# Performance work log

Measured on AMD Instinct MI355X. Metric: run time of the kernel, lower is better.

Reference implementation:

```python
import jax, jax.numpy as jnp
import numpy as np
from jax import lax

# dims: S=seq_len, B=batch, D=word dim, HE=encoder hidden, HD=decoder hidden,
# E=atomic embedding dim, A=num_atomic, T=max_steps, SOS=start token id
S, B, D = 48, 64, 300
HE, HD, E, A, T, SOS = 300, 256, 50, 128, 50, 1


def _u(key, shape, scale):
    return jax.random.uniform(key, shape, jnp.float32, -scale, scale)


def setup_inputs() -> dict:
    key = jax.random.key(0)
    ks = iter(jax.random.split(key, 64))
    inp = {"word_vectors": jax.random.normal(next(ks), (S, B, D), jnp.float32)}
    se = 1.0 / np.sqrt(HE)
    for l, din in ((0, D), (1, 2 * HE)):
        for d in ("f", "b"):
            inp[f"e{l}{d}_Wih"] = _u(next(ks), (3 * HE, din), se)
            inp[f"e{l}{d}_Whh"] = _u(next(ks), (3 * HE, HE), se)
            inp[f"e{l}{d}_bih"] = _u(next(ks), (3 * HE,), se)
            inp[f"e{l}{d}_bhh"] = _u(next(ks), (3 * HE,), se)
    sd = 1.0 / np.sqrt(HD)
    for l, din in ((0, E), (1, HD)):
        inp[f"d{l}_Wih"] = _u(next(ks), (3 * HD, din), sd)
        inp[f"d{l}_Whh"] = _u(next(ks), (3 * HD, HD), sd)
        inp[f"d{l}_bih"] = _u(next(ks), (3 * HD,), sd)
        inp[f"d{l}_bhh"] = _u(next(ks), (3 * HD,), sd)
    emb = jax.random.normal(next(ks), (A, E), jnp.float32)
    inp["emb"] = emb.at[0].set(0.0)  # padding_idx=0
    inp["Wout"] = _u(next(ks), (A, HD), sd)
    inp["bout"] = _u(next(ks), (A,), sd)
    so = 1.0 / np.sqrt(D)
    inp["Wh0"] = _u(next(ks), (2 * HD, D), so)
    inp["bh0"] = _u(next(ks), (2 * HD,), so)
    return inp


def gru_cell(x, h, Wih, Whh, bih, bhh):
    # PyTorch GRU cell semantics
    gi = x @ Wih.T + bih
    gh = h @ Whh.T + bhh
    ir, iz, inn = jnp.split(gi, 3, axis=-1)
    hr, hz, hn = jnp.split(gh, 3, axis=-1)
    r = jax.nn.sigmoid(ir + hr)
    z = jax.nn.sigmoid(iz + hz)
    n = jnp.tanh(inn + r * hn)
    return (1.0 - z) * n + z * h


def gru_layer(xs, Wih, Whh, bih, bhh, reverse=False):
    # xs: [S, B, din] -> [S, B, H]; h0 = zeros (torch default)
    h0 = jnp.zeros((xs.shape[1], Whh.shape[1]), xs.dtype)
    def step(h, x):
        hn = gru_cell(x, h, Wih, Whh, bih, bhh)
        return hn, hn
    _, ys = lax.scan(step, h0, xs, reverse=reverse)
    return ys


def reference(word_vectors, e0f_Wih, e0f_Whh, e0f_bih, e0f_bhh, e0b_Wih, e0b_Whh, e0b_bih, e0b_bhh, e1f_Wih, e1f_Whh, e1f_bih, e1f_bhh, e1b_Wih, e1b_Whh, e1b_bih, e1b_bhh, d0_Wih, d0_Whh, d0_bih, d0_bhh, d1_Wih, d1_Whh, d1_bih, d1_bhh, emb, Wout, bout, Wh0, bh0):
    # --- encoder: 2-layer bidirectional GRU (eval mode: no dropout) ---
    x0f = gru_layer(word_vectors, e0f_Wih, e0f_Whh, e0f_bih, e0f_bhh, reverse=False)
    x0b = gru_layer(word_vectors, e0b_Wih, e0b_Whh, e0b_bih, e0b_bhh, reverse=True)
    x0 = jnp.concatenate([x0f, x0b], axis=-1)  # [S,B,2*HE]
    x1f = gru_layer(x0, e1f_Wih, e1f_Whh, e1f_bih, e1f_bhh, reverse=False)
    x1b = gru_layer(x0, e1b_Wih, e1b_Whh, e1b_bih, e1b_bhh, reverse=True)
    enc = x1f + x1b  # view(S,B,2,HE).sum(dim=2) of concat == sum of directions

    N = S * B
    h = jnp.tanh(enc @ Wh0.T + bh0).reshape(N, 2, HD)  # [N,2,HD]
    h0, h1 = h[:, 0], h[:, 1]
    e = jnp.broadcast_to(emb[SOS], (N, E))

    def step(carry, _):
        h0, h1, e = carry
        h0n = gru_cell(e, h0, d0_Wih, d0_Whh, d0_bih, d0_bhh)
        h1n = gru_cell(h0n, h1, d1_Wih, d1_Whh, d1_bih, d1_bhh)
        y = jax.nn.log_softmax(h1n @ Wout.T + bout, axis=-1)  # [N,A]
        p = jnp.argmax(y, axis=-1)
        return (h0n, h1n, emb[p]), y

    _, Y = lax.scan(step, (h0, h1, e), None, length=T)  # [T,N,A]
    return Y.reshape(T, S, B, A)[:-1]
```

## Files before the change

kernel.cpp:

```cpp
#include <hip/hip_runtime.h>
#include <math.h>

#define S_ 48
#define B_ 64
#define D_ 300
#define HE_ 300
#define HD_ 256
#define E_ 50
#define A_ 128
#define T_ 50
#define N_ (S_*B_)

__device__ __forceinline__ float sigm(float x){ return 1.0f/(1.0f + expf(-x)); }

template<int MODE>
__global__ __launch_bounds__(256)
void gemm_bias_kernel(const float* __restrict__ A, const float* __restrict__ A2,
                      const float* __restrict__ W,
                      const float* __restrict__ bias, float* __restrict__ C,
                      float* __restrict__ C2, int M, int N, int K)
{
  __shared__ float As[16][64];
  __shared__ float Ws[16][64];
  const int tid = threadIdx.x;
  const int bm = blockIdx.y * 64;
  const int bn = blockIdx.x * 64;
  const int tx = tid & 15, ty = tid >> 4;
  const int lr = tid >> 2;
  const int lk = (tid & 3) << 2;
  float acc[4][4] = {{0.f}};
  for (int kb = 0; kb < K; kb += 16) {
    {
      const int row = bm + lr;
      const int k = kb + lk;
      const float* ap = A + (size_t)row * K + k;
      float4 v = make_float4(0.f,0.f,0.f,0.f);
      if (k + 3 < K) v = *reinterpret_cast<const float4*>(ap);
      else {
        if (k   < K) v.x = ap[0];
        if (k+1 < K) v.y = ap[1];
        if (k+2 < K) v.z = ap[2];
        if (k+3 < K) v.w = ap[3];
      }
      if (MODE == 2) {
        const float* ap2 = A2 + (size_t)row * K + k;
        if (k + 3 < K) {
          float4 v2 = *reinterpret_cast<const float4*>(ap2);
          v.x += v2.x; v.y += v2.y; v.z += v2.z; v.w += v2.w;
        } else {
          if (k   < K) v.x += ap2[0];
          if (k+1 < K) v.y += ap2[1];
          if (k+2 < K) v.z += ap2[2];
          if (k+3 < K) v.w += ap2[3];
        }
      }
      As[lk][lr]=v.x; As[lk+1][lr]=v.y; As[lk+2][lr]=v.z; As[lk+3][lr]=v.w;
    }
    {
      const int col = bn + lr;
      const int k = kb + lk;
      float4 v = make_float4(0.f,0.f,0.f,0.f);
      if (col < N) {
        const float* wp = W + (size_t)col * K + k;
        if (k + 3 < K) v = *reinterpret_cast<const float4*>(wp);
        else {
          if (k   < K) v.x = wp[0];
          if (k+1 < K) v.y = wp[1];
          if (k+2 < K) v.z = wp[2];
          if (k+3 < K) v.w = wp[3];
        }
      }
      Ws[lk][lr]=v.x; Ws[lk+1][lr]=v.y; Ws[lk+2][lr]=v.z; Ws[lk+3][lr]=v.w;
    }
    __syncthreads();
    #pragma unroll
    for (int kk = 0; kk < 16; ++kk) {
      float4 a4 = *reinterpret_cast<const float4*>(&As[kk][ty<<2]);
      float4 w4 = *reinterpret_cast<const float4*>(&Ws[kk][tx<<2]);
      const float* a = reinterpret_cast<const float*>(&a4);
      const float* w = reinterpret_cast<const float*>(&w4);
      #pragma unroll
      for (int i = 0; i < 4; ++i)
        #pragma unroll
        for (int j = 0; j < 4; ++j)
          acc[i][j] = fmaf(a[i], w[j], acc[i][j]);
    }
    __syncthreads();
  }
  #pragma unroll
  for (int i = 0; i < 4; ++i) {
    const int m = bm + (ty<<2) + i;
    #pragma unroll
    for (int j = 0; j < 4; ++j) {
      const int n = bn + (tx<<2) + j;
      if (n < N) {
        float v = acc[i][j] + bias[n];
        if (MODE == 0) {
          C[(size_t)m*N + n] = v;
        } else {
          v = tanhf(v);
          if (n < HD_) C[(size_t)m*HD_ + n] = v;
          else         C2[(size_t)m*HD_ + (n-HD_)] = v;
        }
      }
    }
  }
}

__global__ __launch_bounds__(256)
void transpose_kernel(const float* __restrict__ in, float* __restrict__ out,
                      int NC, int NK, int NKP)
{
  int idx = blockIdx.x * 256 + threadIdx.x;
  if (idx < NC*NKP) {
    int cI = idx / NKP, kI = idx % NKP;
    out[(size_t)kI*NC + cI] = (kI < NK) ? in[(size_t)cI*NK + kI] : 0.0f;
  }
}

template<int LAYER>
__global__ __launch_bounds__(640, 2)
void enc_layer_persistent(const float* __restrict__ gi_f, const float* __restrict__ gi_b,
                          const float* __restrict__ WhhT_f, const float* __restrict__ WhhT_b,
                          const float* __restrict__ bhh_f, const float* __restrict__ bhh_b,
                          float* __restrict__ out, float* __restrict__ outB)
{
  const int dir = blockIdx.y;
  const float* gi  = dir ? gi_b   : gi_f;
  const float* WT  = dir ? WhhT_b : WhhT_f;
  const float* bhh = dir ? bhh_b  : bhh_f;
  float* o = (LAYER == 1 && dir) ? outB : out;

  __shared__ float hA[4][304];
  __shared__ float hB[4][304];
  const int tid = threadIdx.x;
  const int half = tid / 320;
  const int j = tid - half*320;
  const int R0 = blockIdx.x * 4;
  const int r0 = half * 2;
  const bool act = (j < HE_);

  float b_r = 0.f, b_z = 0.f, b_n = 0.f;
  if (act) { b_r = bhh[j]; b_z = bhh[HE_+j]; b_n = bhh[2*HE_+j]; }
  __syncthreads();

  for (int t = 0; t < S_; ++t) {
    const int tt = dir ? (S_-1 - t) : t;
    float (*hin)[304]  = (t & 1) ? hB : hA;
    float (*hout)[304] = (t & 1) ? hA : hB;
    float ar[2]={0,0}, az[2]={0,0}, an[2]={0,0};
    if (act && t > 0) {
      for (int k = 0; k < HE_; k += 4) {
        float wr[4], wz[4], wn[4];
        #pragma unroll
        for (int u = 0; u < 4; ++u) {
          const float* wk = WT + (size_t)(k+u)*(3*HE_);
          wr[u] = wk[j]; wz[u] = wk[HE_+j]; wn[u] = wk[2*HE_+j];
        }
        #pragma unroll
        for (int r = 0; r < 2; ++r) {
          float4 h4 = *reinterpret_cast<const float4*>(&hin[r0+r][k]);
          ar[r]=fmaf(h4.x,wr[0],ar[r]); ar[r]=fmaf(h4.y,wr[1],ar[r]);
          ar[r]=fmaf(h4.z,wr[2],ar[r]); ar[r]=fmaf(h4.w,wr[3],ar[r]);
          az[r]=fmaf(h4.x,wz[0],az[r]); az[r]=fmaf(h4.y,wz[1],az[r]);
          az[r]=fmaf(h4.z,wz[2],az[r]); az[r]=fmaf(h4.w,wz[3],az[r]);
          an[r]=fmaf(h4.x,wn[0],an[r]); an[r]=fmaf(h4.y,wn[1],an[r]);
          an[r]=fmaf(h4.z,wn[2],an[r]); an[r]=fmaf(h4.w,wn[3],an[r]);
        }
      }
    }
    if (act) {
      #pragma unroll
      for (int r = 0; r < 2; ++r) {
        const int row = R0 + r0 + r;
        const size_t gb = (size_t)(tt*B_ + row) * (3*HE_);
        float gr = gi[gb + j];
        float gz = gi[gb + HE_ + j];
        float gn = gi[gb + 2*HE_ + j];
        float rg = sigm(gr + ar[r] + b_r);
        float zg = sigm(gz + az[r] + b_z);
        float ng = tanhf(gn + rg*(an[r] + b_n));
        float ho = (t > 0) ? hin[r0+r][j] : 0.0f;
        float hn = (1.0f - zg)*ng + zg*ho;
        hout[r0+r][j] = hn;
        if (LAYER == 0) o[(size_t)(tt*B_ + row)*(2*HE_) + dir*HE_ + j] = hn;
        else            o[(size_t)(tt*B_ + row)*HE_ + j] = hn;
      }
    }
    __syncthreads();
  }
}

__global__ __launch_bounds__(1024, 4)
void dec_persistent(const float* __restrict__ WihT0,
                    const float* __restrict__ WhhT0,
                    const float* __restrict__ WihT1,
                    const float* __restrict__ WhhT1,
                    const float* __restrict__ WoutT,
                    const float* __restrict__ bih0, const float* __restrict__ bhh0,
                    const float* __restrict__ bih1, const float* __restrict__ bhh1,
                    const float* __restrict__ bout,
                    const float* __restrict__ emb,
                    const float* __restrict__ h0init, const float* __restrict__ h1init,
                    float* __restrict__ Y)
{
  __shared__ float h0s[12][256];
  __shared__ float h1s[12][256];
  __shared__ float es[12][52];
  const int tid = threadIdx.x;
  const int R0 = blockIdx.x * 12;
  const int c  = tid & 255;
  const int q  = tid >> 8;
  const int r0 = q * 3;

  for (int i = tid; i < 12*64; i += 1024) {
    int r = i >> 6, k = (i & 63) << 2;
    *reinterpret_cast<float4*>(&h0s[r][k]) =
        *reinterpret_cast<const float4*>(&h0init[(size_t)(R0+r)*HD_ + k]);
    *reinterpret_cast<float4*>(&h1s[r][k]) =
        *reinterpret_cast<const float4*>(&h1init[(size_t)(R0+r)*HD_ + k]);
  }
  for (int i = tid; i < 12*52; i += 1024) {
    int r = i / 52, k = i - r*52;
    es[r][k] = (k < E_) ? emb[E_ + k] : 0.0f;
  }
  const float b0r = bih0[c] + bhh0[c];
  const float b0z = bih0[HD_+c] + bhh0[HD_+c];
  const float b0ni = bih0[2*HD_+c];
  const float b0nh = bhh0[2*HD_+c];
  const float b1r = bih1[c] + bhh1[c];
  const float b1z = bih1[HD_+c] + bhh1[HD_+c];
  const float b1ni = bih1[2*HD_+c];
  const float b1nh = bhh1[2*HD_+c];
  const float bo0 = bout[tid & 63];
  const float bo1 = bout[64 + (tid & 63)];
  __syncthreads();

  for (int s = 0; s < T_-1; ++s) {
    float ar[3]={0,0,0}, az[3]={0,0,0}, ani[3]={0,0,0}, anh[3]={0,0,0};
    for (int kq = 0; kq < 64; ++kq) {
      const int k = kq << 2;
      float wr[4], wz[4], wn[4];
      #pragma unroll
      for (int u = 0; u < 4; ++u) {
        const float* wk = WhhT0 + (size_t)(k+u)*768;
        wr[u]=wk[c]; wz[u]=wk[256+c]; wn[u]=wk[512+c];
      }
      #pragma unroll
      for (int r = 0; r < 3; ++r) {
        float4 x = *reinterpret_cast<const float4*>(&h0s[r0+r][k]);
        ar[r]=fmaf(x.x,wr[0],ar[r]); ar[r]=fmaf(x.y,wr[1],ar[r]);
        ar[r]=fmaf(x.z,wr[2],ar[r]); ar[r]=fmaf(x.w,wr[3],ar[r]);
        az[r]=fmaf(x.x,wz[0],az[r]); az[r]=fmaf(x.y,wz[1],az[r]);
        az[r]=fmaf(x.z,wz[2],az[r]); az[r]=fmaf(x.w,wz[3],az[r]);
        anh[r]=fmaf(x.x,wn[0],anh[r]); anh[r]=fmaf(x.y,wn[1],anh[r]);
        anh[r]=fmaf(x.z,wn[2],anh[r]); anh[r]=fmaf(x.w,wn[3],anh[r]);
      }
      if (kq < 13) {
        float vr[4], vz[4], vn[4];
        #pragma unroll
        for (int u = 0; u < 4; ++u) {
          const float* wk = WihT0 + (size_t)(k+u)*768;
          vr[u]=wk[c]; vz[u]=wk[256+c]; vn[u]=wk[512+c];
        }
        #pragma unroll
        for (int r = 0; r < 3; ++r) {
          float4 e = *reinterpret_cast<const float4*>(&es[r0+r][k]);
          ar[r]=fmaf(e.x,vr[0],ar[r]); ar[r]=fmaf(e.y,vr[1],ar[r]);
          ar[r]=fmaf(e.z,vr[2],ar[r]); ar[r]=fmaf(e.w,vr[3],ar[r]);
          az[r]=fmaf(e.x,vz[0],az[r]); az[r]=fmaf(e.y,vz[1],az[r]);
          az[r]=fmaf(e.z,vz[2],az[r]); az[r]=fmaf(e.w,vz[3],az[r]);
          ani[r]=fmaf(e.x,vn[0],ani[r]); ani[r]=fmaf(e.y,vn[1],ani[r]);
          ani[r]=fmaf(e.z,vn[2],ani[r]); ani[r]=fmaf(e.w,vn[3],ani[r]);
        }
      }
    }
    __syncthreads();
    {
      float hnew[3];
      #pragma unroll
      for (int r = 0; r < 3; ++r) {
        float rg = sigm(ar[r] + b0r);
        float zg = sigm(az[r] + b0z);
        float ng = tanhf(ani[r] + b0ni + rg*(anh[r] + b0nh));
        float hold = h0s[r0+r][c];
        hnew[r] = (1.0f - zg)*ng + zg*hold;
      }
      #pragma unroll
      for (int r = 0; r < 3; ++r) h0s[r0+r][c] = hnew[r];
    }
    __syncthreads();
    #pragma unroll
    for (int r = 0; r < 3; ++r) { ar[r]=0.f; az[r]=0.f; ani[r]=0.f; anh[r]=0.f; }
    for (int kq = 0; kq < 64; ++kq) {
      const int k = kq << 2;
      float vr[4], vz[4], vn[4], wr[4], wz[4], wn[4];
      #pragma unroll
      for (int u = 0; u < 4; ++u) {
        const float* wk  = WihT1 + (size_t)(k+u)*768;
        vr[u]=wk[c]; vz[u]=wk[256+c]; vn[u]=wk[512+c];
        const float* wk2 = WhhT1 + (size_t)(k+u)*768;
        wr[u]=wk2[c]; wz[u]=wk2[256+c]; wn[u]=wk2[512+c];
      }
      #pragma unroll
      for (int r = 0; r < 3; ++r) {
        float4 x = *reinterpret_cast<const float4*>(&h0s[r0+r][k]);
        ar[r]=fmaf(x.x,vr[0],ar[r]); ar[r]=fmaf(x.y,vr[1],ar[r]);
        ar[r]=fmaf(x.z,vr[2],ar[r]); ar[r]=fmaf(x.w,vr[3],ar[r]);
        az[r]=fmaf(x.x,vz[0],az[r]); az[r]=fmaf(x.y,vz[1],az[r]);
        az[r]=fmaf(x.z,vz[2],az[r]); az[r]=fmaf(x.w,vz[3],az[r]);
        ani[r]=fmaf(x.x,vn[0],ani[r]); ani[r]=fmaf(x.y,vn[1],ani[r]);
        ani[r]=fmaf(x.z,vn[2],ani[r]); ani[r]=fmaf(x.w,vn[3],ani[r]);
        float4 y = *reinterpret_cast<const float4*>(&h1s[r0+r][k]);
        ar[r]=fmaf(y.x,wr[0],ar[r]); ar[r]=fmaf(y.y,wr[1],ar[r]);
        ar[r]=fmaf(y.z,wr[2],ar[r]); ar[r]=fmaf(y.w,wr[3],ar[r]);
        az[r]=fmaf(y.x,wz[0],az[r]); az[r]=fmaf(y.y,wz[1],az[r]);
        az[r]=fmaf(y.z,wz[2],az[r]); az[r]=fmaf(y.w,wz[3],az[r]);
        anh[r]=fmaf(y.x,wn[0],anh[r]); anh[r]=fmaf(y.y,wn[1],anh[r]);
        anh[r]=fmaf(y.z,wn[2],anh[r]); anh[r]=fmaf(y.w,wn[3],anh[r]);
      }
    }
    __syncthreads();
    {
      float hnew[3];
      #pragma unroll
      for (int r = 0; r < 3; ++r) {
        float rg = sigm(ar[r] + b1r);
        float zg = sigm(az[r] + b1z);
        float ng = tanhf(ani[r] + b1ni + rg*(anh[r] + b1nh));
        float hold = h1s[r0+r][c];
        hnew[r] = (1.0f - zg)*ng + zg*hold;
      }
      #pragma unroll
      for (int r = 0; r < 3; ++r) h1s[r0+r][c] = hnew[r];
    }
    __syncthreads();
    {
      const int w = tid >> 6;
      const int lane = tid & 63;
      if (w < 12) {
        const int row = w;
        float a0 = 0.f, a1 = 0.f;
        for (int k = 0; k < HD_; k += 2) {
          float w00 = WoutT[(size_t)k*A_ + lane];
          float w01 = WoutT[(size_t)k*A_ + 64 + lane];
          float w10 = WoutT[(size_t)(k+1)*A_ + lane];
          float w11 = WoutT[(size_t)(k+1)*A_ + 64 + lane];
          float2 hv = *reinterpret_cast<const float2*>(&h1s[row][k]);
          a0 = fmaf(hv.x, w00, a0); a0 = fmaf(hv.y, w10, a0);
          a1 = fmaf(hv.x, w01, a1); a1 = fmaf(hv.y, w11, a1);
        }
        float v0 = a0 + bo0;
        float v1 = a1 + bo1;
        float mx = fmaxf(v0, v1);
        #pragma unroll
        for (int off = 32; off >= 1; off >>= 1) mx = fmaxf(mx, __shfl_xor(mx, off));
        float sum = expf(v0 - mx) + expf(v1 - mx);
        #pragma unroll
        for (int off = 32; off >= 1; off >>= 1) sum += __shfl_xor(sum, off);
        float lz = mx + logf(sum);
        float* Yr = Y + ((size_t)s*N_ + R0 + row)*A_;
        Yr[lane]      = v0 - lz;
        Yr[64 + lane] = v1 - lz;
        float bv; int bi;
        if (v0 >= v1) { bv = v0; bi = lane; } else { bv = v1; bi = 64 + lane; }
        #pragma unroll
        for (int off = 32; off >= 1; off >>= 1) {
          float ov = __shfl_xor(bv, off);
          int   oi = __shfl_xor(bi, off);
          if (ov > bv || (ov == bv && oi < bi)) { bv = ov; bi = oi; }
        }
        if (lane < E_) es[row][lane] = emb[(size_t)bi*E_ + lane];
      }
    }
    __syncthreads();
  }
}

extern "C" void kernel_launch(void* const* d_in, const int* in_sizes, int n_in,
                              void* d_out, int out_size, void* d_ws, size_t ws_size,
                              hipStream_t stream)
{
  (void)in_sizes; (void)n_in; (void)out_size; (void)ws_size;
  const float* wv      = (const float*)d_in[0];
  const float* e0f_Wih = (const float*)d_in[1];
  const float* e0f_Whh = (const float*)d_in[2];
  const float* e0f_bih = (const float*)d_in[3];
  const float* e0f_bhh = (const float*)d_in[4];
  const float* e0b_Wih = (const float*)d_in[5];
  const float* e0b_Whh = (const float*)d_in[6];
  const float* e0b_bih = (const float*)d_in[7];
  const float* e0b_bhh = (const float*)d_in[8];
  const float* e1f_Wih = (const float*)d_in[9];
  const float* e1f_Whh = (const float*)d_in[10];
  const float* e1f_bih = (const float*)d_in[11];
  const float* e1f_bhh = (const float*)d_in[12];
  const float* e1b_Wih = (const float*)d_in[13];
  const float* e1b_Whh = (const float*)d_in[14];
  const float* e1b_bih = (const float*)d_in[15];
  const float* e1b_bhh = (const float*)d_in[16];
  const float* d0_Wih  = (const float*)d_in[17];
  const float* d0_Whh  = (const float*)d_in[18];
  const float* d0_bih  = (const float*)d_in[19];
  const float* d0_bhh  = (const float*)d_in[20];
  const float* d1_Wih  = (const float*)d_in[21];
  const float* d1_Whh  = (const float*)d_in[22];
  const float* d1_bih  = (const float*)d_in[23];
  const float* d1_bhh  = (const float*)d_in[24];
  const float* emb     = (const float*)d_in[25];
  const float* Wout    = (const float*)d_in[26];
  const float* bout    = (const float*)d_in[27];
  const float* Wh0     = (const float*)d_in[28];
  const float* bh0     = (const float*)d_in[29];

  float* ws = (float*)d_ws;
  float* giA  = ws;
  float* giB  = giA + (size_t)N_*3*HE_;
  float* x0   = giB + (size_t)N_*3*HE_;
  float* eWhT = x0  + (size_t)N_*2*HE_;
  float* eT0f = eWhT;
  float* eT0b = eT0f + (size_t)3*HE_*HE_;
  float* eT1f = eT0b + (size_t)3*HE_*HE_;
  float* eT1b = eT1f + (size_t)3*HE_*HE_;
  float* encF = x0;
  float* encB = x0 + (size_t)N_*HE_;
  float* h0A  = giA;
  float* h1A  = giA + (size_t)N_*HD_;
  float* WihT0 = eWhT;
  float* WhhT0 = WihT0 + (size_t)52*768;
  float* WihT1 = WhhT0 + (size_t)HD_*768;
  float* WhhT1 = WihT1 + (size_t)HD_*768;
  float* WoutT = WhhT1 + (size_t)HD_*768;
  float* Y = (float*)d_out;

  const dim3 blk(256);

  transpose_kernel<<<dim3((3*HE_*HE_+255)/256), blk, 0, stream>>>(e0f_Whh, eT0f, 3*HE_, HE_, HE_);
  transpose_kernel<<<dim3((3*HE_*HE_+255)/256), blk, 0, stream>>>(e0b_Whh, eT0b, 3*HE_, HE_, HE_);
  transpose_kernel<<<dim3((3*HE_*HE_+255)/256), blk, 0, stream>>>(e1f_Whh, eT1f, 3*HE_, HE_, HE_);
  transpose_kernel<<<dim3((3*HE_*HE_+255)/256), blk, 0, stream>>>(e1b_Whh, eT1b, 3*HE_, HE_, HE_);
  gemm_bias_kernel<0><<<dim3(15,48), blk, 0, stream>>>(wv, nullptr, e0f_Wih, e0f_bih, giA, nullptr, N_, 3*HE_, D_);
  gemm_bias_kernel<0><<<dim3(15,48), blk, 0, stream>>>(wv, nullptr, e0b_Wih, e0b_bih, giB, nullptr, N_, 3*HE_, D_);
  enc_layer_persistent<0><<<dim3(16,2), dim3(640), 0, stream>>>(giA, giB, eT0f, eT0b, e0f_bhh, e0b_bhh, x0, nullptr);
  gemm_bias_kernel<0><<<dim3(15,48), blk, 0, stream>>>(x0, nullptr, e1f_Wih, e1f_bih, giA, nullptr, N_, 3*HE_, 2*HE_);
  gemm_bias_kernel<0><<<dim3(15,48), blk, 0, stream>>>(x0, nullptr, e1b_Wih, e1b_bih, giB, nullptr, N_, 3*HE_, 2*HE_);
  enc_layer_persistent<1><<<dim3(16,2), dim3(640), 0, stream>>>(giA, giB, eT1f, eT1b, e1f_bhh, e1b_bhh, encF, encB);
  transpose_kernel<<<dim3((768*52+255)/256),   blk, 0, stream>>>(d0_Wih, WihT0, 3*HD_, E_,  52);
  transpose_kernel<<<dim3((768*256+255)/256),  blk, 0, stream>>>(d0_Whh, WhhT0, 3*HD_, HD_, HD_);
  transpose_kernel<<<dim3((768*256+255)/256),  blk, 0, stream>>>(d1_Wih, WihT1, 3*HD_, HD_, HD_);
  transpose_kernel<<<dim3((768*256+255)/256),  blk, 0, stream>>>(d1_Whh, WhhT1, 3*HD_, HD_, HD_);
  transpose_kernel<<<dim3((128*256+255)/256),  blk, 0, stream>>>(Wout,   WoutT, A_,    HD_, HD_);
  gemm_bias_kernel<2><<<dim3(8,48), blk, 0, stream>>>(encF, encB, Wh0, bh0, h0A, h1A, N_, 2*HD_, HE_);
  dec_persistent<<<dim3(N_/12), dim3(1024), 0, stream>>>(
      WihT0, WhhT0, WihT1, WhhT1, WoutT,
      d0_bih, d0_bhh, d1_bih, d1_bhh, bout,
      emb, h0A, h1A, Y);
}
```

Measured before the change: 7.987 ms.

## Pack decoder weights as float4 along K and double rows per thread

Decoder GRU weights are repacked so each thread fetches four consecutive K values of one gate column with a single 16-byte load, replacing four strided scalar loads. The block shrinks from 1024 to 512 threads and each thread now computes 6 rows instead of 3. This halves global weight traffic per row and reuses each loaded weight across more rows. The cost is more registers per thread and fewer waves per block to hide latency, and the output projection now loops over rows across 8 waves.

```diff
diff --git a/kernel.cpp b/kernel.cpp
--- a/kernel.cpp
+++ b/kernel.cpp
@@ -108,14 +108,32 @@
 }
 
 __global__ __launch_bounds__(256)
-void transpose_kernel(const float* __restrict__ in, float* __restrict__ out,
-                      int NC, int NK, int NKP)
+void ctranspose_kernel(const float* __restrict__ in, float* __restrict__ out,
+                       int NC, int NK, int NKP, int dstride, int row0, int coff)
 {
   int idx = blockIdx.x * 256 + threadIdx.x;
   if (idx < NC*NKP) {
-    int cI = idx / NKP, kI = idx % NKP;
-    out[(size_t)kI*NC + cI] = (kI < NK) ? in[(size_t)cI*NK + kI] : 0.0f;
-  }
+    int gc = idx / NKP, k = idx % NKP;
+    out[(size_t)(row0+k)*dstride + coff + gc] =
+        (k < NK) ? in[(size_t)gc*NK + k] : 0.0f;
+  }
+}
+
+__global__ __launch_bounds__(256)
+void pack4_kernel(const float* __restrict__ W, float4* __restrict__ P,
+                  int NC, int NK, int K4)
+{
+  int idx = blockIdx.x * 256 + threadIdx.x;
+  if (idx >= NC * K4) return;
+  int k4 = idx / NC, gc = idx % NC;
+  int k = k4 << 2;
+  const float* wp = W + (size_t)gc * NK + k;
+  float4 v = make_float4(0.f,0.f,0.f,0.f);
+  if (k   < NK) v.x = wp[0];
+  if (k+1 < NK) v.y = wp[1];
+  if (k+2 < NK) v.z = wp[2];
+  if (k+3 < NK) v.w = wp[3];
+  P[(size_t)k4 * NC + gc] = v;
 }
 
 template<int LAYER>
@@ -191,11 +209,11 @@
   }
 }
 
-__global__ __launch_bounds__(1024, 4)
-void dec_persistent(const float* __restrict__ WihT0,
-                    const float* __restrict__ WhhT0,
-                    const float* __restrict__ WihT1,
-                    const float* __restrict__ WhhT1,
+__global__ __launch_bounds__(512, 2)
+void dec_persistent(const float4* __restrict__ Wih0P,
+                    const float4* __restrict__ Whh0P,
+                    const float4* __restrict__ Wih1P,
+                    const float4* __restrict__ Whh1P,
                     const float* __restrict__ WoutT,
                     const float* __restrict__ bih0, const float* __restrict__ bhh0,
                     const float* __restrict__ bih1, const float* __restrict__ bhh1,
@@ -204,23 +222,25 @@
                     const float* __restrict__ h0init, const float* __restrict__ h1init,
                     float* __restrict__ Y)
 {
-  __shared__ float h0s[12][256];
-  __shared__ float h1s[12][256];
-  __shared__ float es[12][52];
+  __shared__ __align__(16) float h0s[12][256];
+  __shared__ __align__(16) float h1s[12][256];
+  __shared__ __align__(16) float es[12][52];
   const int tid = threadIdx.x;
   const int R0 = blockIdx.x * 12;
   const int c  = tid & 255;
-  const int q  = tid >> 8;
-  const int r0 = q * 3;
-
-  for (int i = tid; i < 12*64; i += 1024) {
+  const int half = tid >> 8;
+  const int r0 = half * 6;
+  const int lane = tid & 63;
+  const int wave = tid >> 6;
+
+  for (int i = tid; i < 12*64; i += 512) {
     int r = i >> 6, k = (i & 63) << 2;
     *reinterpret_cast<float4*>(&h0s[r][k]) =
         *reinterpret_cast<const float4*>(&h0init[(size_t)(R0+r)*HD_ + k]);
     *reinterpret_cast<float4*>(&h1s[r][k]) =
         *reinterpret_cast<const float4*>(&h1init[(size_t)(R0+r)*HD_ + k]);
   }
-  for (int i = tid; i < 12*52; i += 1024) {
+  for (int i = tid; i < 12*52; i += 512) {
     int r = i / 52, k = i - r*52;
     es[r][k] = (k < E_) ? emb[E_ + k] : 0.0f;
   }
@@ -232,54 +252,49 @@
   const float b1z = bih1[HD_+c] + bhh1[HD_+c];
   const float b1ni = bih1[2*HD_+c];
   const float b1nh = bhh1[2*HD_+c];
-  const float bo0 = bout[tid & 63];
-  const float bo1 = bout[64 + (tid & 63)];
+  const float bo0 = bout[lane];
+  const float bo1 = bout[64 + lane];
   __syncthreads();
 
   for (int s = 0; s < T_-1; ++s) {
-    float ar[3]={0,0,0}, az[3]={0,0,0}, ani[3]={0,0,0}, anh[3]={0,0,0};
+    float ar[6]={0,0,0,0,0,0}, az[6]={0,0,0,0,0,0};
+    float ani[6]={0,0,0,0,0,0}, anh[6]={0,0,0,0,0,0};
     for (int kq = 0; kq < 64; ++kq) {
       const int k = kq << 2;
-      float wr[4], wz[4], wn[4];
-      #pragma unroll
-      for (int u = 0; u < 4; ++u) {
-        const float* wk = WhhT0 + (size_t)(k+u)*768;
-        wr[u]=wk[c]; wz[u]=wk[256+c]; wn[u]=wk[512+c];
-      }
-      #pragma unroll
-      for (int r = 0; r < 3; ++r) {
+      float4 wr = Whh0P[kq*768 + c];
+      float4 wz = Whh0P[kq*768 + 256 + c];
+      float4 wn = Whh0P[kq*768 + 512 + c];
+      #pragma unroll
+      for (int r = 0; r < 6; ++r) {
         float4 x = *reinterpret_cast<const float4*>(&h0s[r0+r][k]);
-        ar[r]=fmaf(x.x,wr[0],ar[r]); ar[r]=fmaf(x.y,wr[1],ar[r]);
-        ar[r]=fmaf(x.z,wr[2],ar[r]); ar[r]=fmaf(x.w,wr[3],ar[r]);
-        az[r]=fmaf(x.x,wz[0],az[r]); az[r]=fmaf(x.y,wz[1],az[r]);
-        az[r]=fmaf(x.z,wz[2],az[r]); az[r]=fmaf(x.w,wz[3],az[r]);
-        anh[r]=fmaf(x.x,wn[0],anh[r]); anh[r]=fmaf(x.y,wn[1],anh[r]);
-        anh[r]=fmaf(x.z,wn[2],anh[r]); anh[r]=fmaf(x.w,wn[3],anh[r]);
+        ar[r]=fmaf(x.x,wr.x,ar[r]); ar[r]=fmaf(x.y,wr.y,ar[r]);
+        ar[r]=fmaf(x.z,wr.z,ar[r]); ar[r]=fmaf(x.w,wr.w,ar[r]);
+        az[r]=fmaf(x.x,wz.x,az[r]); az[r]=fmaf(x.y,wz.y,az[r]);
+        az[r]=fmaf(x.z,wz.z,az[r]); az[r]=fmaf(x.w,wz.w,az[r]);
+        anh[r]=fmaf(x.x,wn.x,anh[r]); anh[r]=fmaf(x.y,wn.y,anh[r]);
+        anh[r]=fmaf(x.z,wn.z,anh[r]); anh[r]=fmaf(x.w,wn.w,anh[r]);
       }
       if (kq < 13) {
-        float vr[4], vz[4], vn[4];
+        float4 vr = Wih0P[kq*768 + c];
+        float4 vz = Wih0P[kq*768 + 256 + c];
+        float4 vn = Wih0P[kq*768 + 512 + c];
         #pragma unroll
-        for (int u = 0; u < 4; ++u) {
-          const float* wk = WihT0 + (size_t)(k+u)*768;
-          vr[u]=wk[c]; vz[u]=wk[256+c]; vn[u]=wk[512+c];
-        }
-        #pragma unroll
-        for (int r = 0; r < 3; ++r) {
+        for (int r = 0; r < 6; ++r) {
           float4 e = *reinterpret_cast<const float4*>(&es[r0+r][k]);
-          ar[r]=fmaf(e.x,vr[0],ar[r]); ar[r]=fmaf(e.y,vr[1],ar[r]);
-          ar[r]=fmaf(e.z,vr[2],ar[r]); ar[r]=fmaf(e.w,vr[3],ar[r]);
-          az[r]=fmaf(e.x,vz[0],az[r]); az[r]=fmaf(e.y,vz[1],az[r]);
-          az[r]=fmaf(e.z,vz[2],az[r]); az[r]=fmaf(e.w,vz[3],az[r]);
-          ani[r]=fmaf(e.x,vn[0],ani[r]); ani[r]=fmaf(e.y,vn[1],ani[r]);
-          ani[r]=fmaf(e.z,vn[2],ani[r]); ani[r]=fmaf(e.w,vn[3],ani[r]);
+          ar[r]=fmaf(e.x,vr.x,ar[r]); ar[r]=fmaf(e.y,vr.y,ar[r]);
+          ar[r]=fmaf(e.z,vr.z,ar[r]); ar[r]=fmaf(e.w,vr.w,ar[r]);
+          az[r]=fmaf(e.x,vz.x,az[r]); az[r]=fmaf(e.y,vz.y,az[r]);
+          az[r]=fmaf(e.z,vz.z,az[r]); az[r]=fmaf(e.w,vz.w,az[r]);
+          ani[r]=fmaf(e.x,vn.x,ani[r]); ani[r]=fmaf(e.y,vn.y,ani[r]);
+          ani[r]=fmaf(e.z,vn.z,ani[r]); ani[r]=fmaf(e.w,vn.w,ani[r]);
         }
       }
     }
     __syncthreads();
     {
-      float hnew[3];
-      #pragma unroll
-      for (int r = 0; r < 3; ++r) {
+      float hnew[6];
+      #pragma unroll
+      for (int r = 0; r < 6; ++r) {
         float rg = sigm(ar[r] + b0r);
         float zg = sigm(az[r] + b0z);
         float ng = tanhf(ani[r] + b0ni + rg*(anh[r] + b0nh));
@@ -287,44 +302,42 @@
         hnew[r] = (1.0f - zg)*ng + zg*hold;
       }
       #pragma unroll
-      for (int r = 0; r < 3; ++r) h0s[r0+r][c] = hnew[r];
+      for (int r = 0; r < 6; ++r) h0s[r0+r][c] = hnew[r];
     }
     __syncthreads();
     #pragma unroll
-    for (int r = 0; r < 3; ++r) { ar[r]=0.f; az[r]=0.f; ani[r]=0.f; anh[r]=0.f; }
+    for (int r = 0; r < 6; ++r) { ar[r]=0.f; az[r]=0.f; ani[r]=0.f; anh[r]=0.f; }
     for (int kq = 0; kq < 64; ++kq) {
       const int k = kq << 2;
-      float vr[4], vz[4], vn[4], wr[4], wz[4], wn[4];
-      #pragma unroll
-      for (int u = 0; u < 4; ++u) {
-        const float* wk  = WihT1 + (size_t)(k+u)*768;
-        vr[u]=wk[c]; vz[u]=wk[256+c]; vn[u]=wk[512+c];
-        const float* wk2 = WhhT1 + (size_t)(k+u)*768;
-        wr[u]=wk2[c]; wz[u]=wk2[256+c]; wn[u]=wk2[512+c];
-      }
-      #pragma unroll
-      for (int r = 0; r < 3; ++r) {
+      float4 vr = Wih1P[kq*768 + c];
+      float4 vz = Wih1P[kq*768 + 256 + c];
+      float4 vn = Wih1P[kq*768 + 512 + c];
+      float4 wr = Whh1P[kq*768 + c];
+      float4 wz = Whh1P[kq*768 + 256 + c];
+      float4 wn = Whh1P[kq*768 + 512 + c];
+      #pragma unroll
+      for (int r = 0; r < 6; ++r) {
         float4 x = *reinterpret_cast<const float4*>(&h0s[r0+r][k]);
-        ar[r]=fmaf(x.x,vr[0],ar[r]); ar[r]=fmaf(x.y,vr[1],ar[r]);
-        ar[r]=fmaf(x.z,vr[2],ar[r]); ar[r]=fmaf(x.w,vr[3],ar[r]);
-        az[r]=fmaf(x.x,vz[0],az[r]); az[r]=fmaf(x.y,vz[1],az[r]);
-        az[r]=fmaf(x.z,vz[2],az[r]); az[r]=fmaf(x.w,vz[3],az[r]);
-        ani[r]=fmaf(x.x,vn[0],ani[r]); ani[r]=fmaf(x.y,vn[1],ani[r]);
-        ani[r]=fmaf(x.z,vn[2],ani[r]); ani[r]=fmaf(x.w,vn[3],ani[r]);
+        ar[r]=fmaf(x.x,vr.x,ar[r]); ar[r]=fmaf(x.y,vr.y,ar[r]);
+        ar[r]=fmaf(x.z,vr.z,ar[r]); ar[r]=fmaf(x.w,vr.w,ar[r]);
+        az[r]=fmaf(x.x,vz.x,az[r]); az[r]=fmaf(x.y,vz.y,az[r]);
+        az[r]=fmaf(x.z,vz.z,az[r]); az[r]=fmaf(x.w,vz.w,az[r]);
+        ani[r]=fmaf(x.x,vn.x,ani[r]); ani[r]=fmaf(x.y,vn.y,ani[r]);
+        ani[r]=fmaf(x.z,vn.z,ani[r]); ani[r]=fmaf(x.w,vn.w,ani[r]);
         float4 y = *reinterpret_cast<const float4*>(&h1s[r0+r][k]);
-        ar[r]=fmaf(y.x,wr[0],ar[r]); ar[r]=fmaf(y.y,wr[1],ar[r]);
-        ar[r]=fmaf(y.z,wr[2],ar[r]); ar[r]=fmaf(y.w,wr[3],ar[r]);
-        az[r]=fmaf(y.x,wz[0],az[r]); az[r]=fmaf(y.y,wz[1],az[r]);
-        az[r]=fmaf(y.z,wz[2],az[r]); az[r]=fmaf(y.w,wz[3],az[r]);
-        anh[r]=fmaf(y.x,wn[0],anh[r]); anh[r]=fmaf(y.y,wn[1],anh[r]);
-        anh[r]=fmaf(y.z,wn[2],anh[r]); anh[r]=fmaf(y.w,wn[3],anh[r]);
+        ar[r]=fmaf(y.x,wr.x,ar[r]); ar[r]=fmaf(y.y,wr.y,ar[r]);
+        ar[r]=fmaf(y.z,wr.z,ar[r]); ar[r]=fmaf(y.w,wr.w,ar[r]);
+        az[r]=fmaf(y.x,wz.x,az[r]); az[r]=fmaf(y.y,wz.y,az[r]);
+        az[r]=fmaf(y.z,wz.z,az[r]); az[r]=fmaf(y.w,wz.w,az[r]);
+        anh[r]=fmaf(y.x,wn.x,anh[r]); anh[r]=fmaf(y.y,wn.y,anh[r]);
+        anh[r]=fmaf(y.z,wn.z,anh[r]); anh[r]=fmaf(y.w,wn.w,anh[r]);
       }
     }
     __syncthreads();
     {
-      float hnew[3];
-      #pragma unroll
-      for (int r = 0; r < 3; ++r) {
+      float hnew[6];
+      #pragma unroll
+      for (int r = 0; r < 6; ++r) {
         float rg = sigm(ar[r] + b1r);
         float zg = sigm(az[r] + b1z);
         float ng = tanhf(ani[r] + b1ni + rg*(anh[r] + b1nh));
@@ -332,46 +345,41 @@
         hnew[r] = (1.0f - zg)*ng + zg*hold;
       }
       #pragma unroll
-      for (int r = 0; r < 3; ++r) h1s[r0+r][c] = hnew[r];
-    }
-    __syncthreads();
-    {
-      const int w = tid >> 6;
-      const int lane = tid & 63;
-      if (w < 12) {
-        const int row = w;
-        float a0 = 0.f, a1 = 0.f;
-        for (int k = 0; k < HD_; k += 2) {
-          float w00 = WoutT[(size_t)k*A_ + lane];
-          float w01 = WoutT[(size_t)k*A_ + 64 + lane];
-          float w10 = WoutT[(size_t)(k+1)*A_ + lane];
-          float w11 = WoutT[(size_t)(k+1)*A_ + 64 + lane];
-          float2 hv = *reinterpret_cast<const float2*>(&h1s[row][k]);
-          a0 = fmaf(hv.x, w00, a0); a0 = fmaf(hv.y, w10, a0);
-          a1 = fmaf(hv.x, w01, a1); a1 = fmaf(hv.y, w11, a1);
-        }
-        float v0 = a0 + bo0;
-        float v1 = a1 + bo1;
-        float mx = fmaxf(v0, v1);
-        #pragma unroll
-        for (int off = 32; off >= 1; off >>= 1) mx = fmaxf(mx, __shfl_xor(mx, off));
-        float sum = expf(v0 - mx) + expf(v1 - mx);
-        #pragma unroll
-        for (int off = 32; off >= 1; off >>= 1) sum += __shfl_xor(sum, off);
-        float lz = mx + logf(sum);
-        float* Yr = Y + ((size_t)s*N_ + R0 + row)*A_;
-        Yr[lane]      = v0 - lz;
-        Yr[64 + lane] = v1 - lz;
-        float bv; int bi;
-        if (v0 >= v1) { bv = v0; bi = lane; } else { bv = v1; bi = 64 + lane; }
-        #pragma unroll
-        for (int off = 32; off >= 1; off >>= 1) {
-          float ov = __shfl_xor(bv, off);
-          int   oi = __shfl_xor(bi, off);
-          if (ov > bv || (ov == bv && oi < bi)) { bv = ov; bi = oi; }
-        }
-        if (lane < E_) es[row][lane] = emb[(size_t)bi*E_ + lane];
-      }
+      for (int r = 0; r < 6; ++r) h1s[r0+r][c] = hnew[r];
+    }
+    __syncthreads();
+    for (int rr = wave; rr < 12; rr += 8) {
+      float a0 = 0.f, a1 = 0.f;
+      for (int k = 0; k < HD_; k += 2) {
+        float w00 = WoutT[(size_t)k*A_ + lane];
+        float w01 = WoutT[(size_t)k*A_ + 64 + lane];
+        float w10 = WoutT[(size_t)(k+1)*A_ + lane];
+        float w11 = WoutT[(size_t)(k+1)*A_ + 64 + lane];
+        float2 hv = *reinterpret_cast<const float2*>(&h1s[rr][k]);
+        a0 = fmaf(hv.x, w00, a0); a0 = fmaf(hv.y, w10, a0);
+        a1 = fmaf(hv.x, w01, a1); a1 = fmaf(hv.y, w11, a1);
+      }
+      float v0 = a0 + bo0;
+      float v1 = a1 + bo1;
+      float mx = fmaxf(v0, v1);
+      #pragma unroll
+      for (int off = 32; off >= 1; off >>= 1) mx = fmaxf(mx, __shfl_xor(mx, off));
+      float sum = expf(v0 - mx) + expf(v1 - mx);
+      #pragma unroll
+      for (int off = 32; off >= 1; off >>= 1) sum += __shfl_xor(sum, off);
+      float lz = mx + logf(sum);
+      float* Yr = Y + ((size_t)s*N_ + R0 + rr)*A_;
+      Yr[lane]      = v0 - lz;
+      Yr[64 + lane] = v1 - lz;
+      float bv; int bi;
+      if (v0 >= v1) { bv = v0; bi = lane; } else { bv = v1; bi = 64 + lane; }
+      #pragma unroll
+      for (int off = 32; off >= 1; off >>= 1) {
+        float ov = __shfl_xor(bv, off);
+        int   oi = __shfl_xor(bi, off);
+        if (ov > bv || (ov == bv && oi < bi)) { bv = ov; bi = oi; }
+      }
+      if (lane < E_) es[rr][lane] = emb[(size_t)bi*E_ + lane];
     }
     __syncthreads();
   }
@@ -426,33 +434,33 @@
   float* encB = x0 + (size_t)N_*HE_;
   float* h0A  = giA;
   float* h1A  = giA + (size_t)N_*HD_;
-  float* WihT0 = eWhT;
-  float* WhhT0 = WihT0 + (size_t)52*768;
-  float* WihT1 = WhhT0 + (size_t)HD_*768;
-  float* WhhT1 = WihT1 + (size_t)HD_*768;
-  float* WoutT = WhhT1 + (size_t)HD_*768;
+  float4* Wih0P = (float4*)eWhT;
+  float4* Whh0P = Wih0P + (size_t)13*768;
+  float4* Wih1P = Whh0P + (size_t)64*768;
+  float4* Whh1P = Wih1P + (size_t)64*768;
+  float*  WoutT = (float*)(Whh1P + (size_t)64*768);
   float* Y = (float*)d_out;
 
   const dim3 blk(256);
 
-  transpose_kernel<<<dim3((3*HE_*HE_+255)/256), blk, 0, stream>>>(e0f_Whh, eT0f, 3*HE_, HE_, HE_);
-  transpose_kernel<<<dim3((3*HE_*HE_+255)/256), blk, 0, stream>>>(e0b_Whh, eT0b, 3*HE_, HE_, HE_);
-  transpose_kernel<<<dim3((3*HE_*HE_+255)/256), blk, 0, stream>>>(e1f_Whh, eT1f, 3*HE_, HE_, HE_);
-  transpose_kernel<<<dim3((3*HE_*HE_+255)/256), blk, 0, stream>>>(e1b_Whh, eT1b, 3*HE_, HE_, HE_);
+  ctranspose_kernel<<<dim3(1055), blk, 0, stream>>>(e0f_Whh, eT0f, 3*HE_, HE_, HE_, 3*HE_, 0, 0);
+  ctranspose_kernel<<<dim3(1055), blk, 0, stream>>>(e0b_Whh, eT0b, 3*HE_, HE_, HE_, 3*HE_, 0, 0);
+  ctranspose_kernel<<<dim3(1055), blk, 0, stream>>>(e1f_Whh, eT1f, 3*HE_, HE_, HE_, 3*HE_, 0, 0);
+  ctranspose_kernel<<<dim3(1055), blk, 0, stream>>>(e1b_Whh, eT1b, 3*HE_, HE_, HE_, 3*HE_, 0, 0);
   gemm_bias_kernel<0><<<dim3(15,48), blk, 0, stream>>>(wv, nullptr, e0f_Wih, e0f_bih, giA, nullptr, N_, 3*HE_, D_);
   gemm_bias_kernel<0><<<dim3(15,48), blk, 0, stream>>>(wv, nullptr, e0b_Wih, e0b_bih, giB, nullptr, N_, 3*HE_, D_);
   enc_layer_persistent<0><<<dim3(16,2), dim3(640), 0, stream>>>(giA, giB, eT0f, eT0b, e0f_bhh, e0b_bhh, x0, nullptr);
   gemm_bias_kernel<0><<<dim3(15,48), blk, 0, stream>>>(x0, nullptr, e1f_Wih, e1f_bih, giA, nullptr, N_, 3*HE_, 2*HE_);
   gemm_bias_kernel<0><<<dim3(15,48), blk, 0, stream>>>(x0, nullptr, e1b_Wih, e1b_bih, giB, nullptr, N_, 3*HE_, 2*HE_);
   enc_layer_persistent<1><<<dim3(16,2), dim3(640), 0, stream>>>(giA, giB, eT1f, eT1b, e1f_bhh, e1b_bhh, encF, encB);
-  transpose_kernel<<<dim3((768*52+255)/256),   blk, 0, stream>>>(d0_Wih, WihT0, 3*HD_, E_,  52);
-  transpose_kernel<<<dim3((768*256+255)/256),  blk, 0, stream>>>(d0_Whh, WhhT0, 3*HD_, HD_, HD_);
-  transpose_kernel<<<dim3((768*256+255)/256),  blk, 0, stream>>>(d1_Wih, WihT1, 3*HD_, HD_, HD_);
-  transpose_kernel<<<dim3((768*256+255)/256),  blk, 0, stream>>>(d1_Whh, WhhT1, 3*HD_, HD_, HD_);
-  transpose_kernel<<<dim3((128*256+255)/256),  blk, 0, stream>>>(Wout,   WoutT, A_,    HD_, HD_);
+  pack4_kernel<<<dim3(39),  blk, 0, stream>>>(d0_Wih, Wih0P, 3*HD_, E_,  13);
+  pack4_kernel<<<dim3(192), blk, 0, stream>>>(d0_Whh, Whh0P, 3*HD_, HD_, 64);
+  pack4_kernel<<<dim3(192), blk, 0, stream>>>(d1_Wih, Wih1P, 3*HD_, HD_, 64);
+  pack4_kernel<<<dim3(192), blk, 0, stream>>>(d1_Whh, Whh1P, 3*HD_, HD_, 64);
+  ctranspose_kernel<<<dim3(128), blk, 0, stream>>>(Wout, WoutT, A_, HD_, HD_, 128, 0, 0);
   gemm_bias_kernel<2><<<dim3(8,48), blk, 0, stream>>>(encF, encB, Wh0, bh0, h0A, h1A, N_, 2*HD_, HE_);
-  dec_persistent<<<dim3(N_/12), dim3(1024), 0, stream>>>(
-      WihT0, WhhT0, WihT1, WhhT1, WoutT,
+  dec_persistent<<<dim3(N_/12), dim3(512), 0, stream>>>(
+      Wih0P, Whh0P, Wih1P, Whh1P, WoutT,
       d0_bih, d0_bhh, d1_bih, d1_bhh, bout,
       emb, h0A, h1A, Y);
 }
```

Result: faster. 7.015 ms (-12.2%).
